# Optimization experiments

Measured on AMD Instinct MI355X. Metric: run time of the kernel, lower is better.

Reference implementation:

```python
import jax, jax.numpy as jnp
import numpy as np

B, T, E, H = 2, 4096, 1024, 16
SEGS = (256, 512, 1024, 2048, 4096)
DILS = (1, 2, 4, 8, 16)
NEG = -1e8  # torchscale uses -1e8 for uncovered / masked lse entries


def setup_inputs() -> dict:
    key = jax.random.key(0)
    ks = jax.random.split(key, 5)
    sc = 0.02
    zb = jnp.zeros((E,), jnp.float32)
    return {
        "x": jax.random.normal(ks[0], (B, T, E), jnp.float32),
        "wq": jax.random.normal(ks[1], (E, E), jnp.float32) * sc,
        "bq": zb,
        "wk": jax.random.normal(ks[2], (E, E), jnp.float32) * sc,
        "bk": zb,
        "wv": jax.random.normal(ks[3], (E, E), jnp.float32) * sc,
        "bv": zb,
        "wo": jax.random.normal(ks[4], (E, E), jnp.float32) * sc,
        "bo": zb,
    }


def _scale_attn(q, k, v, w, r):
    # One LongNet scale: segment length w, dilation ratio r.
    # Head group g = head // (H//r) attends to in-segment positions p with p % r == g
    # (torchscale dense_to_sparse diagonal over (r1, r2)).
    Bq, Tq, Hq, d = q.shape
    n, s, hp = Tq // w, w // r, Hq // r  # segments, sparse length, heads per group

    def gather(x):
        # [B,T,H,d] -> segments [B,n,w,H,d]; split w=(s,r1) (p=l*r+r1) and H=(r2,hp);
        # keep diagonal r1 == r2.
        x = x.reshape(Bq, n, s, r, r, hp, d)
        x = jnp.diagonal(x, axis1=3, axis2=4)          # [B,n,s,hp,d,r]
        return jnp.moveaxis(x, -1, 3).reshape(Bq, n, s, Hq, d)

    qs, ks_, vs = gather(q), gather(k), gather(v)
    scores = jnp.einsum('bnqhd,bnkhd->bnhqk', qs, ks_)
    mask = jnp.tril(jnp.ones((s, s), dtype=bool))       # causal within sparse segment
    scores = jnp.where(mask, scores, NEG)
    lse = jax.scipy.special.logsumexp(scores, axis=-1)  # [B,n,h,q]
    out = jnp.einsum('bnhqk,bnkhd->bnqhd', jax.nn.softmax(scores, axis=-1), vs)

    # Scatter back to dense positions (sparse_to_dense): uncovered -> out 0, lse -1e8.
    eye = jnp.eye(r, dtype=out.dtype)
    out_g = out.reshape(Bq, n, s, r, hp, d)                               # heads as (g, hp)
    dense = jnp.einsum('bnsghd,pg->bnspghd', out_g, eye).reshape(Bq, Tq, Hq, d)
    lse_g = jnp.transpose(lse, (0, 1, 3, 2)).reshape(Bq, n, s, r, hp)     # [B,n,s,g,hp]
    lse_d = jnp.where(eye[:, :, None] > 0, lse_g[:, :, :, None, :, :], NEG)
    return dense, lse_d.reshape(Bq, Tq, Hq)


def reference(x, wq, bq, wk, bk, wv, bv, wo, bo):
    d = E // H
    q = (x @ wq + bq).reshape(B, T, H, d) * (d ** -0.5)
    k = (x @ wk + bk).reshape(B, T, H, d)
    v = (x @ wv + bv).reshape(B, T, H, d)
    outs, lses = [], []
    for w_, r_ in zip(SEGS, DILS):
        o, l = _scale_attn(q, k, v, w_, r_)
        outs.append(o)
        lses.append(l)
    # Merge scales with softmax over per-scale log-sum-exp (dense-attention equivalence).
    wgt = jax.nn.softmax(jnp.stack(lses), axis=0)[..., None]  # [S,B,T,H,1]
    y = jnp.sum(jnp.stack(outs) * wgt, axis=0).reshape(B, T, E)
    return y @ wo + bo
```

## Files before the change

### kernel.cpp

```cpp
#include <hip/hip_runtime.h>
#include <hip/hip_bf16.h>

typedef __bf16 bf16_t;
typedef __bf16 bf16x8 __attribute__((ext_vector_type(8)));
typedef __bf16 bf16x4 __attribute__((ext_vector_type(4)));
typedef float f32x4 __attribute__((ext_vector_type(4)));
typedef int vint4 __attribute__((ext_vector_type(4)));

#define AS1 __attribute__((address_space(1)))
#define AS3 __attribute__((address_space(3)))

constexpr int B_ = 2, T_ = 4096, E_ = 1024, H_ = 16;
constexpr int M_ = B_ * T_;

__device__ constexpr size_t OB_OFF[5]  = {0, 8388608, 12582912, 14680064, 15728640};
__device__ constexpr size_t LSE_OFF[5] = {0, 131072, 196608, 229376, 245760};
constexpr size_t OB_TOTAL  = 16252928;
constexpr size_t LSE_TOTAL = 253952;

__global__ __launch_bounds__(256) void cvt_f32_bf16(const float* __restrict__ in,
                                                    bf16_t* __restrict__ out) {
  int i = (blockIdx.x * 256 + threadIdx.x) * 4;
  const float4 v = *(const float4*)(in + i);
  bf16x4 o;
  o[0] = (bf16_t)v.x; o[1] = (bf16_t)v.y; o[2] = (bf16_t)v.z; o[3] = (bf16_t)v.w;
  *(bf16x4*)(out + i) = o;
}

__global__ __launch_bounds__(256) void cvt_transpose_w(
    const float* __restrict__ w0, const float* __restrict__ w1,
    const float* __restrict__ w2, const float* __restrict__ w3,
    bf16_t* __restrict__ o0, bf16_t* __restrict__ o1,
    bf16_t* __restrict__ o2, bf16_t* __restrict__ o3) {
  __shared__ float tile[32][33];
  const float* src; bf16_t* dst;
  switch (blockIdx.z) {
    case 0: src = w0; dst = o0; break;
    case 1: src = w1; dst = o1; break;
    case 2: src = w2; dst = o2; break;
    default: src = w3; dst = o3; break;
  }
  const int n0 = blockIdx.x * 32, k0 = blockIdx.y * 32;
  const int tx = threadIdx.x & 31, ty = threadIdx.x >> 5;
#pragma unroll
  for (int i = 0; i < 32; i += 8)
    tile[ty + i][tx] = src[(size_t)(k0 + ty + i) * E_ + n0 + tx];
  __syncthreads();
#pragma unroll
  for (int i = 0; i < 32; i += 8)
    dst[(size_t)(n0 + ty + i) * E_ + k0 + tx] = (bf16_t)tile[tx][ty + i];
}

template <bool OUT_BF16, bool QKV>
__global__ __launch_bounds__(256, 4) void gemm_bt(
    const bf16_t* __restrict__ A, const bf16_t* __restrict__ BT,
    const float* __restrict__ bias0, const float* __restrict__ bias1,
    const float* __restrict__ bias2, void* __restrict__ Cout, float qscale) {
  constexpr int K = E_;
  __shared__ bf16_t As[128 * 64];
  __shared__ bf16_t Bs[128 * 64];
  const int tid = threadIdx.x;
  const int lane = tid & 63;
  const int wave = tid >> 6;
  const int wm = wave >> 1, wn = wave & 1;
  const int lc = lane & 15, lg = lane >> 4;
  const int bm = blockIdx.x;
  int bn = blockIdx.y;

  const float* bias = bias0;
  float scale = 1.0f;
  void* outp = Cout;
  const bf16_t* Bt = BT;
  if (QKV) {
    const int which = bn >> 3;
    bn &= 7;
    bias = (which == 0) ? bias0 : (which == 1) ? bias1 : bias2;
    scale = (which == 0) ? qscale : 1.0f;
    outp = (void*)((bf16_t*)Cout + (size_t)which * M_ * E_);
    Bt += (size_t)which * E_ * E_;
  }

  f32x4 acc[4][4] = {};

  const int lrow = tid >> 3;
  const int schunk = (tid & 7) ^ (lrow & 7);
  const bf16_t* Ag = A + (size_t)(bm * 128 + lrow) * K + schunk * 8;
  const bf16_t* Bg = Bt + (size_t)(bn * 128 + lrow) * K + schunk * 8;

  const int sl0 = ((0 * 4 + lg) ^ (lc & 7)) * 8;
  const int sl1 = ((1 * 4 + lg) ^ (lc & 7)) * 8;

  for (int k0 = 0; k0 < K; k0 += 64) {
    __syncthreads();
#pragma unroll
    for (int p = 0; p < 4; ++p) {
      __builtin_amdgcn_global_load_lds(
          (const AS1 void*)(Ag + (size_t)(p * 32) * K + k0),
          (AS3 void*)(As + p * 2048 + tid * 8), 16, 0, 0);
      __builtin_amdgcn_global_load_lds(
          (const AS1 void*)(Bg + (size_t)(p * 32) * K + k0),
          (AS3 void*)(Bs + p * 2048 + tid * 8), 16, 0, 0);
    }
    __syncthreads();
#pragma unroll
    for (int kk = 0; kk < 2; ++kk) {
      const int sl = kk ? sl1 : sl0;
      bf16x8 af[4], bfr[4];
#pragma unroll
      for (int i = 0; i < 4; ++i) {
        af[i]  = *(const bf16x8*)&As[(wm * 64 + i * 16 + lc) * 64 + sl];
        bfr[i] = *(const bf16x8*)&Bs[(wn * 64 + i * 16 + lc) * 64 + sl];
      }
#pragma unroll
      for (int i = 0; i < 4; ++i)
#pragma unroll
        for (int j = 0; j < 4; ++j)
          acc[i][j] = __builtin_amdgcn_mfma_f32_16x16x32_bf16(af[i], bfr[j], acc[i][j], 0, 0, 0);
    }
  }

#pragma unroll
  for (int i = 0; i < 4; ++i) {
    const int row = bm * 128 + wm * 64 + i * 16 + lg * 4;
#pragma unroll
    for (int j = 0; j < 4; ++j) {
      const int col = bn * 128 + wn * 64 + j * 16 + lc;
      const float bv = bias[col];
#pragma unroll
      for (int rg = 0; rg < 4; ++rg) {
        const float v = (acc[i][j][rg] + bv) * scale;
        if (OUT_BF16)
          ((bf16_t*)outp)[(size_t)(row + rg) * E_ + col] = (bf16_t)v;
        else
          ((float*)outp)[(size_t)(row + rg) * E_ + col] = v;
      }
    }
  }
}

__global__ __launch_bounds__(512, 4) void attn_inst(
    const bf16_t* __restrict__ Q, const bf16_t* __restrict__ K,
    const bf16_t* __restrict__ V, bf16_t* __restrict__ Ob,
    float* __restrict__ Lse) {
  __shared__ alignas(16) bf16_t Ks[256][72];
  __shared__ alignas(16) bf16_t Vt[64][264];
  __shared__ alignas(16) bf16_t Pw[8][16][40];

  const int bid = blockIdx.x;
  int s, ibase;
  if (bid < 512)      { s = 0; ibase = 0; }
  else if (bid < 768) { s = 1; ibase = 512; }
  else if (bid < 896) { s = 2; ibase = 768; }
  else if (bid < 960) { s = 3; ibase = 896; }
  else                { s = 4; ibase = 960; }
  const int inst = bid - ibase;
  const int h = inst & 15;
  const int nseg_log = 4 - s;
  const int seg = (inst >> 4) & ((1 << nseg_log) - 1);
  const int b = inst >> (4 + nseg_log);
  const int g = h >> (4 - s);

  const int t = threadIdx.x;
  const int lane = t & 63;
  const int wv = t >> 6;
  const int lc = lane & 15;
  const int lg = lane >> 4;

  {
    const int row = t >> 1, ch = (t & 1) * 32;
    const int tk = ((seg * 256 + row) << s) + g;
    const size_t off = ((size_t)b * T_ + tk) * E_ + h * 64 + ch;
    const bf16_t* Kg = K + off;
    const bf16_t* Vg = V + off;
#pragma unroll
    for (int j = 0; j < 4; ++j)
      *(bf16x8*)&Ks[row][ch + j * 8] = *(const bf16x8*)(Kg + j * 8);
#pragma unroll
    for (int j = 0; j < 4; ++j) {
      bf16x8 va = *(const bf16x8*)(Vg + j * 8);
#pragma unroll
      for (int e = 0; e < 8; ++e) Vt[ch + j * 8 + e][row] = va[e];
    }
  }
  __syncthreads();

  const size_t rowbase = (size_t)(b * H_ + h) * (T_ >> s) + seg * 256;

#pragma unroll
  for (int sel = 0; sel < 2; ++sel) {
    const int tile = sel ? (15 - wv) : wv;
    const int q = tile * 16 + lc;

    const int tq = ((seg * 256 + q) << s) + g;
    const bf16_t* Qg = Q + ((size_t)b * T_ + tq) * E_ + h * 64 + lg * 8;
    bf16x8 qfrag0 = *(const bf16x8*)(Qg);
    bf16x8 qfrag1 = *(const bf16x8*)(Qg + 32);

    float m = -INFINITY, Z = 0.0f;
    f32x4 Oa[4] = {};

    const int nkb = tile / 4 + 1;
    const int diag = tile / 4;
    for (int kb = 0; kb < nkb; ++kb) {
      f32x4 sacc[4] = {};
      __builtin_amdgcn_s_setprio(1);
#pragma unroll
      for (int kt = 0; kt < 4; ++kt) {
        bf16x8 kf0 = *(const bf16x8*)&Ks[kb * 64 + kt * 16 + lc][lg * 8];
        bf16x8 kf1 = *(const bf16x8*)&Ks[kb * 64 + kt * 16 + lc][32 + lg * 8];
        sacc[kt] = __builtin_amdgcn_mfma_f32_16x16x32_bf16(kf0, qfrag0, sacc[kt], 0, 0, 0);
        sacc[kt] = __builtin_amdgcn_mfma_f32_16x16x32_bf16(kf1, qfrag1, sacc[kt], 0, 0, 0);
      }
      __builtin_amdgcn_s_setprio(0);
      if (kb == diag) {
#pragma unroll
        for (int kt = 0; kt < 4; ++kt)
#pragma unroll
          for (int rg = 0; rg < 4; ++rg)
            if (kb * 64 + kt * 16 + lg * 4 + rg > q) sacc[kt][rg] = -1e30f;
      }
      float pm = -1e30f;
#pragma unroll
      for (int kt = 0; kt < 4; ++kt) {
        pm = fmaxf(pm, fmaxf(fmaxf(sacc[kt][0], sacc[kt][1]),
                             fmaxf(sacc[kt][2], sacc[kt][3])));
      }
      pm = fmaxf(pm, __shfl_xor(pm, 16));
      pm = fmaxf(pm, __shfl_xor(pm, 32));
      if (!__all(pm - m <= 11.5f)) {
        const float nm = fmaxf(m, pm);
        const float crr = __builtin_amdgcn_exp2f(m - nm);
        Z *= crr;
#pragma unroll
        for (int dt = 0; dt < 4; ++dt)
#pragma unroll
          for (int rg = 0; rg < 4; ++rg) Oa[dt][rg] *= crr;
        m = nm;
      }
      float psum = 0.0f;
      bf16x4 pv[4];
#pragma unroll
      for (int kt = 0; kt < 4; ++kt)
#pragma unroll
        for (int rg = 0; rg < 4; ++rg) {
          const float p = __builtin_amdgcn_exp2f(sacc[kt][rg] - m);
          psum += p;
          pv[kt][rg] = (bf16_t)p;
        }
      psum += __shfl_xor(psum, 16);
      psum += __shfl_xor(psum, 32);
      Z += psum;
#pragma unroll
      for (int hf = 0; hf < 2; ++hf) {
        *(bf16x4*)&Pw[wv][lc][lg * 4]      = pv[hf * 2 + 0];
        *(bf16x4*)&Pw[wv][lc][16 + lg * 4] = pv[hf * 2 + 1];
        bf16x8 pb = *(const bf16x8*)&Pw[wv][lc][lg * 8];
        __builtin_amdgcn_s_setprio(1);
#pragma unroll
        for (int dt = 0; dt < 4; ++dt) {
          bf16x8 vf = *(const bf16x8*)&Vt[dt * 16 + lc][(kb * 2 + hf) * 32 + lg * 8];
          Oa[dt] = __builtin_amdgcn_mfma_f32_16x16x32_bf16(vf, pb, Oa[dt], 0, 0, 0);
        }
        __builtin_amdgcn_s_setprio(0);
      }
    }

    const float lse = m + __builtin_amdgcn_logf(Z);
    const float iZ = 1.0f / Z;
    bf16_t* orow = Ob + OB_OFF[s] + (rowbase + q) * 64 + lg * 4;
#pragma unroll
    for (int dt = 0; dt < 4; ++dt) {
      bf16x4 ov;
      ov[0] = (bf16_t)(Oa[dt][0] * iZ);
      ov[1] = (bf16_t)(Oa[dt][1] * iZ);
      ov[2] = (bf16_t)(Oa[dt][2] * iZ);
      ov[3] = (bf16_t)(Oa[dt][3] * iZ);
      *(bf16x4*)(orow + dt * 16) = ov;
    }
    if (lg == 0) Lse[LSE_OFF[s] + rowbase + q] = lse;
  }
}

__global__ __launch_bounds__(256) void attn_merge(const bf16_t* __restrict__ Ob,
                                                  const float* __restrict__ Lse,
                                                  bf16_t* __restrict__ Y) {
  const int gtid = blockIdx.x * 256 + threadIdx.x;
  const int d8 = gtid & 7;
  const int h = (gtid >> 3) & 15;
  const int tt = (gtid >> 7) & (T_ - 1);
  const int b = gtid >> 19;

  float m = -INFINITY, S = 0.0f;
  float acc[8];
#pragma unroll
  for (int j = 0; j < 8; ++j) acc[j] = 0.0f;

#pragma unroll
  for (int s = 0; s < 5; ++s) {
    const int r = 1 << s;
    const int g = h >> (4 - s);
    if ((tt & (r - 1)) != g) continue;
    const size_t idx = (size_t)(b * H_ + h) * (T_ >> s) + (tt >> s);
    const float lse = Lse[LSE_OFF[s] + idx];
    const bf16x8 ov = *(const bf16x8*)(Ob + OB_OFF[s] + idx * 64 + d8 * 8);
    const float nM = fmaxf(m, lse);
    const float a = __builtin_amdgcn_exp2f(m - nM);
    const float e = __builtin_amdgcn_exp2f(lse - nM);
#pragma unroll
    for (int j = 0; j < 8; ++j) acc[j] = acc[j] * a + (float)ov[j] * e;
    S = S * a + e;
    m = nM;
  }

  const float invS = 1.0f / S;
  bf16x8 o;
#pragma unroll
  for (int j = 0; j < 8; ++j) o[j] = (bf16_t)(acc[j] * invS);
  *(bf16x8*)(Y + (size_t)gtid * 8) = o;
}

extern "C" void kernel_launch(void* const* d_in, const int* in_sizes, int n_in,
                              void* d_out, int out_size, void* d_ws, size_t ws_size,
                              hipStream_t stream) {
  (void)in_sizes; (void)n_in; (void)out_size; (void)ws_size;
  const float* x  = (const float*)d_in[0];
  const float* wq = (const float*)d_in[1];
  const float* bq = (const float*)d_in[2];
  const float* wk = (const float*)d_in[3];
  const float* bk = (const float*)d_in[4];
  const float* wv = (const float*)d_in[5];
  const float* bv = (const float*)d_in[6];
  const float* wo = (const float*)d_in[7];
  const float* bo = (const float*)d_in[8];

  char* p = (char*)d_ws;
  auto take = [&](size_t bytes) {
    char* q = p;
    p += (bytes + 255) & ~(size_t)255;
    return (void*)q;
  };
  bf16_t* wq_t = (bf16_t*)take((size_t)E_ * E_ * 2);
  bf16_t* wk_t = (bf16_t*)take((size_t)E_ * E_ * 2);
  bf16_t* wv_t = (bf16_t*)take((size_t)E_ * E_ * 2);
  bf16_t* wo_t = (bf16_t*)take((size_t)E_ * E_ * 2);
  bf16_t* xb   = (bf16_t*)take((size_t)M_ * E_ * 2);
  bf16_t* qb   = (bf16_t*)take((size_t)M_ * E_ * 2);
  bf16_t* kbuf = (bf16_t*)take((size_t)M_ * E_ * 2);
  bf16_t* vbuf = (bf16_t*)take((size_t)M_ * E_ * 2);
  bf16_t* yb   = (bf16_t*)take((size_t)M_ * E_ * 2);
  bf16_t* Ob   = (bf16_t*)take(OB_TOTAL * 2);
  float*  Lse  = (float*)take(LSE_TOTAL * 4);
  (void)wk_t; (void)wv_t;

  cvt_f32_bf16<<<M_ * E_ / 1024, 256, 0, stream>>>(x, xb);
  cvt_transpose_w<<<dim3(32, 32, 4), 256, 0, stream>>>(wq, wk, wv, wo, wq_t, wk_t, wv_t, wo_t);

  gemm_bt<true, true><<<dim3(M_ / 128, 24), 256, 0, stream>>>(
      xb, wq_t, bq, bk, bv, qb, 0.125f * 1.44269504f);

  attn_inst<<<992, 512, 0, stream>>>(qb, kbuf, vbuf, Ob, Lse);

  attn_merge<<<M_ * E_ / 8 / 256, 256, 0, stream>>>(Ob, Lse, yb);

  gemm_bt<false, false><<<dim3(M_ / 128, 8), 256, 0, stream>>>(
      yb, wo_t, bo, bo, bo, d_out, 1.0f);
}
```

Before: 130.8 us.

## Fuse scale merge into scale-0 attention launch after dilated scales

Splits attention into two launches. The first computes the dilated scales 1-4 and writes their partial outputs and LSE. The second computes scale 0 and merges it in registers with the stored partials, writing Y directly, so the separate merge kernel and the scale-0 round trip to global memory go away. In exchange the single 992-block launch becomes two serialized launches, which can leave the GPU underfilled in the smaller first launch and lose overlap across scales.

```diff
diff --git a/kernel.cpp b/kernel.cpp
--- a/kernel.cpp
+++ b/kernel.cpp
@@ -138,21 +138,22 @@
   }
 }
 
+template <bool S0>
 __global__ __launch_bounds__(512, 4) void attn_inst(
     const bf16_t* __restrict__ Q, const bf16_t* __restrict__ K,
     const bf16_t* __restrict__ V, bf16_t* __restrict__ Ob,
-    float* __restrict__ Lse) {
+    float* __restrict__ Lse, bf16_t* __restrict__ Y) {
   __shared__ alignas(16) bf16_t Ks[256][72];
   __shared__ alignas(16) bf16_t Vt[64][264];
   __shared__ alignas(16) bf16_t Pw[8][16][40];
 
   const int bid = blockIdx.x;
   int s, ibase;
-  if (bid < 512)      { s = 0; ibase = 0; }
-  else if (bid < 768) { s = 1; ibase = 512; }
-  else if (bid < 896) { s = 2; ibase = 768; }
-  else if (bid < 960) { s = 3; ibase = 896; }
-  else                { s = 4; ibase = 960; }
+  if (S0) { s = 0; ibase = 0; }
+  else if (bid < 256) { s = 1; ibase = 0; }
+  else if (bid < 384) { s = 2; ibase = 256; }
+  else if (bid < 448) { s = 3; ibase = 384; }
+  else                { s = 4; ibase = 448; }
   const int inst = bid - ibase;
   const int h = inst & 15;
   const int nseg_log = 4 - s;
@@ -267,56 +268,60 @@
 
     const float lse = m + __builtin_amdgcn_logf(Z);
     const float iZ = 1.0f / Z;
-    bf16_t* orow = Ob + OB_OFF[s] + (rowbase + q) * 64 + lg * 4;
-#pragma unroll
-    for (int dt = 0; dt < 4; ++dt) {
-      bf16x4 ov;
-      ov[0] = (bf16_t)(Oa[dt][0] * iZ);
-      ov[1] = (bf16_t)(Oa[dt][1] * iZ);
-      ov[2] = (bf16_t)(Oa[dt][2] * iZ);
-      ov[3] = (bf16_t)(Oa[dt][3] * iZ);
-      *(bf16x4*)(orow + dt * 16) = ov;
-    }
-    if (lg == 0) Lse[LSE_OFF[s] + rowbase + q] = lse;
-  }
-}
-
-__global__ __launch_bounds__(256) void attn_merge(const bf16_t* __restrict__ Ob,
-                                                  const float* __restrict__ Lse,
-                                                  bf16_t* __restrict__ Y) {
-  const int gtid = blockIdx.x * 256 + threadIdx.x;
-  const int d8 = gtid & 7;
-  const int h = (gtid >> 3) & 15;
-  const int tt = (gtid >> 7) & (T_ - 1);
-  const int b = gtid >> 19;
-
-  float m = -INFINITY, S = 0.0f;
-  float acc[8];
-#pragma unroll
-  for (int j = 0; j < 8; ++j) acc[j] = 0.0f;
-
-#pragma unroll
-  for (int s = 0; s < 5; ++s) {
-    const int r = 1 << s;
-    const int g = h >> (4 - s);
-    if ((tt & (r - 1)) != g) continue;
-    const size_t idx = (size_t)(b * H_ + h) * (T_ >> s) + (tt >> s);
-    const float lse = Lse[LSE_OFF[s] + idx];
-    const bf16x8 ov = *(const bf16x8*)(Ob + OB_OFF[s] + idx * 64 + d8 * 8);
-    const float nM = fmaxf(m, lse);
-    const float a = __builtin_amdgcn_exp2f(m - nM);
-    const float e = __builtin_amdgcn_exp2f(lse - nM);
-#pragma unroll
-    for (int j = 0; j < 8; ++j) acc[j] = acc[j] * a + (float)ov[j] * e;
-    S = S * a + e;
-    m = nM;
-  }
-
-  const float invS = 1.0f / S;
-  bf16x8 o;
-#pragma unroll
-  for (int j = 0; j < 8; ++j) o[j] = (bf16_t)(acc[j] * invS);
-  *(bf16x8*)(Y + (size_t)gtid * 8) = o;
+    if (!S0) {
+      bf16_t* orow = Ob + OB_OFF[s] + (rowbase + q) * 64 + lg * 4;
+#pragma unroll
+      for (int dt = 0; dt < 4; ++dt) {
+        bf16x4 ov;
+        ov[0] = (bf16_t)(Oa[dt][0] * iZ);
+        ov[1] = (bf16_t)(Oa[dt][1] * iZ);
+        ov[2] = (bf16_t)(Oa[dt][2] * iZ);
+        ov[3] = (bf16_t)(Oa[dt][3] * iZ);
+        *(bf16x4*)(orow + dt * 16) = ov;
+      }
+      if (lg == 0) Lse[LSE_OFF[s] + rowbase + q] = lse;
+    } else {
+      const int t_glob = seg * 256 + q;
+      float o16[4][4];
+#pragma unroll
+      for (int dt = 0; dt < 4; ++dt)
+#pragma unroll
+        for (int rg = 0; rg < 4; ++rg) o16[dt][rg] = Oa[dt][rg] * iZ;
+      float M = lse, S = 1.0f;
+#pragma unroll
+      for (int s2 = 1; s2 <= 4; ++s2) {
+        const int r = 1 << s2;
+        const int gg = h >> (4 - s2);
+        if ((t_glob & (r - 1)) != gg) continue;
+        const size_t idx = (size_t)(b * H_ + h) * (T_ >> s2) + (t_glob >> s2);
+        const float l2 = Lse[LSE_OFF[s2] + idx];
+        const bf16_t* orow = Ob + OB_OFF[s2] + idx * 64 + lg * 4;
+        const float nM = fmaxf(M, l2);
+        const float a = __builtin_amdgcn_exp2f(M - nM);
+        const float e = __builtin_amdgcn_exp2f(l2 - nM);
+#pragma unroll
+        for (int dt = 0; dt < 4; ++dt) {
+          const bf16x4 ov = *(const bf16x4*)(orow + dt * 16);
+#pragma unroll
+          for (int rg = 0; rg < 4; ++rg)
+            o16[dt][rg] = o16[dt][rg] * a + (float)ov[rg] * e;
+        }
+        S = S * a + e;
+        M = nM;
+      }
+      const float invS = 1.0f / S;
+      bf16_t* yrow = Y + ((size_t)b * T_ + t_glob) * E_ + h * 64 + lg * 4;
+#pragma unroll
+      for (int dt = 0; dt < 4; ++dt) {
+        bf16x4 ov;
+        ov[0] = (bf16_t)(o16[dt][0] * invS);
+        ov[1] = (bf16_t)(o16[dt][1] * invS);
+        ov[2] = (bf16_t)(o16[dt][2] * invS);
+        ov[3] = (bf16_t)(o16[dt][3] * invS);
+        *(bf16x4*)(yrow + dt * 16) = ov;
+      }
+    }
+  }
 }
 
 extern "C" void kernel_launch(void* const* d_in, const int* in_sizes, int n_in,
@@ -358,9 +363,8 @@
   gemm_bt<true, true><<<dim3(M_ / 128, 24), 256, 0, stream>>>(
       xb, wq_t, bq, bk, bv, qb, 0.125f * 1.44269504f);
 
-  attn_inst<<<992, 512, 0, stream>>>(qb, kbuf, vbuf, Ob, Lse);
-
-  attn_merge<<<M_ * E_ / 8 / 256, 256, 0, stream>>>(Ob, Lse, yb);
+  attn_inst<false><<<480, 512, 0, stream>>>(qb, kbuf, vbuf, Ob, Lse, yb);
+  attn_inst<true><<<512, 512, 0, stream>>>(qb, kbuf, vbuf, Ob, Lse, yb);
 
   gemm_bt<false, false><<<dim3(M_ / 128, 8), 256, 0, stream>>>(
       yb, wo_t, bo, bo, bo, d_out, 1.0f);
```

After: 126.4 us (median of 2 runs). -3.4%, faster.
